# Optimization experiments

Hardware: AMD Instinct MI355X
Metric: run time of the kernel (lower is better)

The kernel has to match this reference:

```python
import jax, jax.numpy as jnp
import numpy as np

B, S, E, H = 2, 2048, 1024, 16
DH = E // H  # 64
EPS = 1e-5


def layer_norm(x, g, b):
    mu = jnp.mean(x, axis=-1, keepdims=True)
    var = jnp.mean(jnp.square(x - mu), axis=-1, keepdims=True)
    return (x - mu) * jax.lax.rsqrt(var + EPS) * g + b


def setup_inputs() -> dict:
    key = jax.random.key(0)
    ks = jax.random.split(key, 12)
    s = lambda fan_in: 1.0 / np.sqrt(fan_in)
    return {
        "x": jax.random.normal(ks[0], (B, S, E), dtype=jnp.float32),
        "ln1_g": jnp.ones((E,), jnp.float32),
        "ln1_b": jnp.zeros((E,), jnp.float32),
        # per-head projections, batched over head axis: [H, E, DH]
        "Wq": jax.random.uniform(ks[1], (H, E, DH), jnp.float32, -s(E), s(E)),
        "Wk": jax.random.uniform(ks[2], (H, E, DH), jnp.float32, -s(E), s(E)),
        "Wv": jax.random.uniform(ks[3], (H, E, DH), jnp.float32, -s(E), s(E)),
        "Wo": jax.random.uniform(ks[4], (H * DH, E), jnp.float32, -s(H * DH), s(H * DH)),
        "bo": jax.random.uniform(ks[5], (E,), jnp.float32, -s(H * DH), s(H * DH)),
        "ln2_g": jnp.ones((E,), jnp.float32),
        "ln2_b": jnp.zeros((E,), jnp.float32),
        "W1": jax.random.uniform(ks[6], (E, 4 * E), jnp.float32, -s(E), s(E)),
        "b1": jax.random.uniform(ks[7], (4 * E,), jnp.float32, -s(E), s(E)),
        "W2": jax.random.uniform(ks[8], (4 * E, E), jnp.float32, -s(4 * E), s(4 * E)),
        "b2": jax.random.uniform(ks[9], (E,), jnp.float32, -s(4 * E), s(4 * E)),
    }


def reference(x, ln1_g, ln1_b, Wq, Wk, Wv, Wo, bo, ln2_g, ln2_b, W1, b1, W2, b2):
    b, s, e = x.shape
    # --- multi-head attention (pre-LN) ---
    h = layer_norm(x, ln1_g, ln1_b)
    q = jnp.einsum("bse,hed->bhsd", h, Wq)
    k = jnp.einsum("bse,hed->bhsd", h, Wk)
    v = jnp.einsum("bse,hed->bhsd", h, Wv)
    # NOTE: original scales by channel**-0.5 (embed_size), not head_size
    scores = jnp.einsum("bhsd,bhtd->bhst", q, k) * (e ** -0.5)
    causal = jnp.tril(jnp.ones((s, s), dtype=bool))
    scores = jnp.where(causal, scores, -jnp.inf)
    attn = jax.nn.softmax(scores, axis=-1)  # dropout is identity in eval
    out = jnp.einsum("bhst,bhtd->bhsd", attn, v)
    out = out.transpose(0, 2, 1, 3).reshape(b, s, -1)  # concat heads: [B,S,H*DH]
    x = x + out @ Wo + bo
    # --- feed-forward (pre-LN) ---
    h2 = layer_norm(x, ln2_g, ln2_b)
    ff = jax.nn.relu(h2 @ W1 + b1) @ W2 + b2
    return x + ff
```

## Files before the change

kernel.cpp:

```cpp
#include <hip/hip_runtime.h>


typedef __bf16 bf16_t;
typedef __attribute__((ext_vector_type(8))) __bf16 bf16x8;
typedef __attribute__((ext_vector_type(4))) __bf16 bf16x4;
typedef __attribute__((ext_vector_type(4))) float f32x4;

#define B_DIM 2
#define S_DIM 2048
#define E_DIM 1024
#define H_DIM 16
#define DH_DIM 64

#define GLD16(gp, lp) __builtin_amdgcn_global_load_lds( \
    (const __attribute__((address_space(1))) void*)(gp), \
    (__attribute__((address_space(3))) void*)(lp), 16, 0, 0)

#define Q_SCALE 0.0450842120f

__global__ __launch_bounds__(256) void ln_kernel(
    const float* __restrict__ x, const float* __restrict__ g,
    const float* __restrict__ bv, bf16_t* __restrict__ out)
{
  const int row = blockIdx.x;
  const int t = threadIdx.x;
  const float* xr = x + (size_t)row * E_DIM;
  float4 v = *(const float4*)&xr[t * 4];
  float s  = v.x + v.y + v.z + v.w;
  float s2 = v.x*v.x + v.y*v.y + v.z*v.z + v.w*v.w;
#pragma unroll
  for (int m = 1; m < 64; m <<= 1) {
    s  += __shfl_xor(s,  m, 64);
    s2 += __shfl_xor(s2, m, 64);
  }
  __shared__ float red[8];
  const int wid = t >> 6, lane = t & 63;
  if (lane == 0) { red[wid] = s; red[4 + wid] = s2; }
  __syncthreads();
  s  = red[0] + red[1] + red[2] + red[3];
  s2 = red[4] + red[5] + red[6] + red[7];
  const float mu  = s * (1.f / E_DIM);
  const float var = s2 * (1.f / E_DIM) - mu * mu;
  const float rs  = rsqrtf(var + 1e-5f);
  float4 gg = *(const float4*)&g[t * 4];
  float4 bb = *(const float4*)&bv[t * 4];
  bf16x4 o;
  o[0] = (bf16_t)((v.x - mu) * rs * gg.x + bb.x);
  o[1] = (bf16_t)((v.y - mu) * rs * gg.y + bb.y);
  o[2] = (bf16_t)((v.z - mu) * rs * gg.z + bb.z);
  o[3] = (bf16_t)((v.w - mu) * rs * gg.w + bb.w);
  *(bf16x4*)&out[(size_t)row * E_DIM + t * 4] = o;
}

__global__ __launch_bounds__(256) void reduce2_ln(
    const float* __restrict__ p, const float* __restrict__ bo,
    const float* __restrict__ x, const float* __restrict__ g,
    const float* __restrict__ bv, float* __restrict__ xmid, bf16_t* __restrict__ h2)
{
  const int row = blockIdx.x;
  const int t = threadIdx.x;
  const size_t off = (size_t)row * E_DIM + t * 4;
  float4 a  = *(const float4*)&p[off];
  float4 b4 = *(const float4*)&p[(size_t)4096 * E_DIM + off];
  float4 xr = *(const float4*)&x[off];
  float4 bo4 = *(const float4*)&bo[t * 4];
  float4 v;
  v.x = a.x + b4.x + xr.x + bo4.x;
  v.y = a.y + b4.y + xr.y + bo4.y;
  v.z = a.z + b4.z + xr.z + bo4.z;
  v.w = a.w + b4.w + xr.w + bo4.w;
  *(float4*)&xmid[off] = v;
  float s  = v.x + v.y + v.z + v.w;
  float s2 = v.x*v.x + v.y*v.y + v.z*v.z + v.w*v.w;
#pragma unroll
  for (int m = 1; m < 64; m <<= 1) {
    s  += __shfl_xor(s,  m, 64);
    s2 += __shfl_xor(s2, m, 64);
  }
  __shared__ float red[8];
  const int wid = t >> 6, lane = t & 63;
  if (lane == 0) { red[wid] = s; red[4 + wid] = s2; }
  __syncthreads();
  s  = red[0] + red[1] + red[2] + red[3];
  s2 = red[4] + red[5] + red[6] + red[7];
  const float mu  = s * (1.f / E_DIM);
  const float var = s2 * (1.f / E_DIM) - mu * mu;
  const float rs  = rsqrtf(var + 1e-5f);
  float4 gg = *(const float4*)&g[t * 4];
  float4 bb = *(const float4*)&bv[t * 4];
  bf16x4 o;
  o[0] = (bf16_t)((v.x - mu) * rs * gg.x + bb.x);
  o[1] = (bf16_t)((v.y - mu) * rs * gg.y + bb.y);
  o[2] = (bf16_t)((v.z - mu) * rs * gg.z + bb.z);
  o[3] = (bf16_t)((v.w - mu) * rs * gg.w + bb.w);
  *(bf16x4*)&h2[off] = o;
}

__global__ __launch_bounds__(256) void reduce4(
    const bf16_t* __restrict__ p0, const bf16_t* __restrict__ p1,
    const bf16_t* __restrict__ p2, const bf16_t* __restrict__ p3,
    const float* __restrict__ b2, const float* __restrict__ xm,
    float* __restrict__ out)
{
  const int row = blockIdx.x;
  const int t = threadIdx.x;
  const size_t off = (size_t)row * E_DIM + t * 4;
  bf16x4 a0 = *(const bf16x4*)&p0[off];
  bf16x4 a1 = *(const bf16x4*)&p1[off];
  bf16x4 a2 = *(const bf16x4*)&p2[off];
  bf16x4 a3 = *(const bf16x4*)&p3[off];
  float4 xr = *(const float4*)&xm[off];
  float4 bb = *(const float4*)&b2[t * 4];
  float4 o;
  o.x = (float)a0[0] + (float)a1[0] + (float)a2[0] + (float)a3[0] + xr.x + bb.x;
  o.y = (float)a0[1] + (float)a1[1] + (float)a2[1] + (float)a3[1] + xr.y + bb.y;
  o.z = (float)a0[2] + (float)a1[2] + (float)a2[2] + (float)a3[2] + xr.z + bb.z;
  o.w = (float)a0[3] + (float)a1[3] + (float)a2[3] + (float)a3[3] + xr.w + bb.w;
  *(float4*)&out[off] = o;
}

__global__ __launch_bounds__(256) void transpose_cast(
    const float* __restrict__ src, bf16_t* __restrict__ dst, int R, int C)
{
  __shared__ float tile[64][65];
  const int c0 = blockIdx.x * 64, r0 = blockIdx.y * 64;
  const int t = threadIdx.x;
  const int rr = t >> 2;
#pragma unroll
  for (int u = 0; u < 4; u++) {
    const int cc = (t & 3) * 4 + u * 16;
    float4 f = *(const float4*)&src[(size_t)(r0 + rr) * C + c0 + cc];
    tile[rr][cc + 0] = f.x; tile[rr][cc + 1] = f.y;
    tile[rr][cc + 2] = f.z; tile[rr][cc + 3] = f.w;
  }
  __syncthreads();
  const int oc = t >> 2;
#pragma unroll
  for (int u = 0; u < 4; u++) {
    const int orr = (t & 3) * 4 + u * 16;
    bf16x4 w;
    w[0] = (bf16_t)tile[orr + 0][oc];
    w[1] = (bf16_t)tile[orr + 1][oc];
    w[2] = (bf16_t)tile[orr + 2][oc];
    w[3] = (bf16_t)tile[orr + 3][oc];
    *(bf16x4*)&dst[(size_t)(c0 + oc) * R + r0 + orr] = w;
  }
}

__global__ __launch_bounds__(256) void qkv_transpose(
    const float* __restrict__ Wq, const float* __restrict__ Wk,
    const float* __restrict__ Wv, bf16_t* __restrict__ dstT)
{
  const int m = blockIdx.y >> 4, h = blockIdx.y & 15;
  const float* src = (m == 0 ? Wq : (m == 1 ? Wk : Wv)) + (size_t)h * E_DIM * DH_DIM;
  const int e0 = blockIdx.x * 64;
  __shared__ float tile[64][65];
  const int t = threadIdx.x;
  const int rr = t >> 2;
#pragma unroll
  for (int u = 0; u < 4; u++) {
    const int cc = (t & 3) * 4 + u * 16;
    float4 f = *(const float4*)&src[(size_t)(e0 + rr) * DH_DIM + cc];
    tile[rr][cc + 0] = f.x; tile[rr][cc + 1] = f.y;
    tile[rr][cc + 2] = f.z; tile[rr][cc + 3] = f.w;
  }
  __syncthreads();
  const int oc = t >> 2;
  const size_t drow = (size_t)(m * 1024 + h * 64 + oc) * E_DIM;
#pragma unroll
  for (int u = 0; u < 4; u++) {
    const int orr = (t & 3) * 4 + u * 16;
    bf16x4 w;
    w[0] = (bf16_t)tile[orr + 0][oc];
    w[1] = (bf16_t)tile[orr + 1][oc];
    w[2] = (bf16_t)tile[orr + 2][oc];
    w[3] = (bf16_t)tile[orr + 3][oc];
    *(bf16x4*)&dstT[drow + e0 + orr] = w;
  }
}

constexpr int EPI_QKV = 0, EPI_BIAS_RELU = 2, EPI_PART_F32 = 3, EPI_PART_B16 = 4;


template <int EPI>
__global__ __launch_bounds__(256) void gemm128_kernel(
    const bf16_t* __restrict__ A, const bf16_t* __restrict__ Bt,
    int M, int N, int Kst, int Klen,
    const float* __restrict__ bias,
    float* __restrict__ outF, bf16_t* __restrict__ outB,
    bf16_t* __restrict__ qo, bf16_t* __restrict__ ko, bf16_t* __restrict__ vo)
{
  __shared__ bf16_t As[3][128 * 32];
  __shared__ bf16_t Bs[3][128 * 32];
  const int gx = gridDim.x;
  const int nwg = gx * gridDim.y;
  int id = blockIdx.y * gx + blockIdx.x;
  id = (id & 7) * (nwg >> 3) + (id >> 3);
  const int m0 = (id % gx) * 128, n0 = (id / gx) * 128;
  const int sp = blockIdx.z;
  A  += (size_t)sp * Klen;
  Bt += (size_t)sp * Klen;

  const int tid = threadIdx.x, lane = tid & 63, wid = tid >> 6;
  const int wr = wid >> 1, wc = wid & 1;
  const int lr = lane & 15, lg = lane >> 4;
  const int halfr = lr >> 1;
  const int sl16 = (((lr & 1) * 4 + lg) ^ halfr) * 16;
  const int baseA = (wr * 32 + halfr) * 128 + sl16;
  const int baseB = (wc * 32 + halfr) * 128 + sl16;

  auto stage = [&](int kt, int buf) {
#pragma unroll
    for (int p = 0; p < 2; p++) {
      const int L = p * 256 + tid;
      const int row2 = L >> 3;
      const int s = (L & 7) ^ (row2 & 7);
      const int r = row2 * 2 + (s >> 2);
      const int u = s & 3;
      char* lb = (char*)&As[buf][0] + (size_t)(p * 256 + wid * 64) * 16;
      char* lbB = (char*)&Bs[buf][0] + (size_t)(p * 256 + wid * 64) * 16;
      GLD16(A  + (size_t)(m0 + r) * Kst + kt * 32 + u * 8, lb);
      GLD16(Bt + (size_t)(n0 + r) * Kst + kt * 32 + u * 8, lbB);
    }
  };

  const f32x4 z4 = {0.f, 0.f, 0.f, 0.f};
  f32x4 acc[4][4];
#pragma unroll
  for (int i = 0; i < 4; i++)
#pragma unroll
    for (int j = 0; j < 4; j++) acc[i][j] = z4;

  const int NT = Klen / 32;
  stage(0, 0);
  stage(1, 1);
  for (int T = 0; T < NT; ++T) {
    const int b = T % 3;
    if (T + 1 < NT) asm volatile("s_waitcnt vmcnt(4)" ::: "memory");
    else            asm volatile("s_waitcnt vmcnt(0)" ::: "memory");
    __builtin_amdgcn_s_barrier();
    if (T + 2 < NT) stage(T + 2, (T + 2) % 3);
    __builtin_amdgcn_sched_barrier(0);

    bf16x8 af[4], bfr[4];
#pragma unroll
    for (int j = 0; j < 4; j++)
      bfr[j] = *(const bf16x8*)((const char*)&Bs[b][0] + baseB + j * 1024);
#pragma unroll
    for (int i = 0; i < 4; i++)
      af[i] = *(const bf16x8*)((const char*)&As[b][0] + baseA + i * 1024);
    __builtin_amdgcn_s_setprio(1);
#pragma unroll
    for (int i = 0; i < 4; i++)
#pragma unroll
      for (int j = 0; j < 4; j++)
        acc[i][j] = __builtin_amdgcn_mfma_f32_16x16x32_bf16(af[i], bfr[j], acc[i][j], 0, 0, 0);
    __builtin_amdgcn_s_setprio(0);
  }

#pragma unroll
  for (int i = 0; i < 4; i++) {
#pragma unroll
    for (int j = 0; j < 4; j++) {
#pragma unroll
      for (int r = 0; r < 4; r++) {
        const int m = m0 + wr * 64 + i * 16 + lg * 4 + r;
        const int n = n0 + wc * 64 + j * 16 + lr;
        const float val = acc[i][j][r];
        if constexpr (EPI == EPI_QKV) {
          const int tsel = n >> 10, h = (n >> 6) & 15, d = n & 63;
          const int b_ = m >> 11, s_ = m & 2047;
          if (tsel == 0)
            qo[((size_t)((b_ * H_DIM + h) * S_DIM + s_)) * DH_DIM + d] = (bf16_t)(val * Q_SCALE);
          else if (tsel == 1)
            ko[((size_t)((b_ * H_DIM + h) * S_DIM + s_)) * DH_DIM + d] = (bf16_t)val;
          else
            vo[((size_t)((b_ * H_DIM + h) * DH_DIM + d)) * S_DIM + s_] = (bf16_t)val;
        } else if constexpr (EPI == EPI_BIAS_RELU) {
          const float u = val + bias[n];
          outB[(size_t)m * N + n] = (bf16_t)(u > 0.f ? u : 0.f);
        } else if constexpr (EPI == EPI_PART_F32) {
          outF[(size_t)sp * M * N + (size_t)m * N + n] = val;
        } else {
          bf16_t* o = sp == 0 ? outB : sp == 1 ? qo : sp == 2 ? ko : vo;
          o[(size_t)m * N + n] = (bf16_t)val;
        }
      }
    }
  }
}

template <int EPI>
__global__ __launch_bounds__(512, 2) void gemm256_kernel(
    const bf16_t* __restrict__ A, const bf16_t* __restrict__ Bt,
    int M, int N, int Kst, int Klen,
    const float* __restrict__ bias,
    float* __restrict__ outF, bf16_t* __restrict__ outB,
    bf16_t* __restrict__ qo, bf16_t* __restrict__ ko, bf16_t* __restrict__ vo)
{
  __shared__ bf16_t As[3][256 * 32];
  __shared__ bf16_t Bs[3][256 * 32];
  const int gx = gridDim.x;
  const int nwg = gx * gridDim.y;
  int id = blockIdx.y * gx + blockIdx.x;
  id = (id & 7) * (nwg >> 3) + (id >> 3);
  const int m0 = (id % gx) * 256, n0 = (id / gx) * 256;
  const int sp = blockIdx.z;
  A  += (size_t)sp * Klen;
  Bt += (size_t)sp * Klen;

  const int tid = threadIdx.x, lane = tid & 63, wid = tid >> 6;
  const int wm = wid >> 2, wn = wid & 3;
  const int lr = lane & 15, lg = lane >> 4;
  const int halfr = lr >> 1;
  const int sl16 = (((lr & 1) * 4 + lg) ^ halfr) * 16;
  const int baseA = (wm * 64 + halfr) * 128 + sl16;
  const int baseB = (wn * 32 + halfr) * 128 + sl16;

  auto stage = [&](int kt, int buf) {
#pragma unroll
    for (int p = 0; p < 2; p++) {
      const int L = p * 512 + tid;
      const int row2 = L >> 3;
      const int s = (L & 7) ^ (row2 & 7);
      const int r = row2 * 2 + (s >> 2);
      const int u = s & 3;
      char* lb = (char*)&As[buf][0] + (size_t)(p * 512 + wid * 64) * 16;
      char* lbB = (char*)&Bs[buf][0] + (size_t)(p * 512 + wid * 64) * 16;
      GLD16(A  + (size_t)(m0 + r) * Kst + kt * 32 + u * 8, lb);
      GLD16(Bt + (size_t)(n0 + r) * Kst + kt * 32 + u * 8, lbB);
    }
  };

  const f32x4 z4 = {0.f, 0.f, 0.f, 0.f};
  f32x4 acc[8][4];
#pragma unroll
  for (int i = 0; i < 8; i++)
#pragma unroll
    for (int j = 0; j < 4; j++) acc[i][j] = z4;

  const int NT = Klen / 32;
  stage(0, 0);
  stage(1, 1);
  for (int T = 0; T < NT; ++T) {
    const int b = T % 3;
    if (T + 1 < NT) asm volatile("s_waitcnt vmcnt(4)" ::: "memory");
    else            asm volatile("s_waitcnt vmcnt(0)" ::: "memory");
    __builtin_amdgcn_s_barrier();
    if (T + 2 < NT) stage(T + 2, (T + 2) % 3);
    __builtin_amdgcn_sched_barrier(0);

    bf16x8 bfr[4];
#pragma unroll
    for (int j = 0; j < 4; j++)
      bfr[j] = *(const bf16x8*)((const char*)&Bs[b][0] + baseB + j * 1024);
    __builtin_amdgcn_s_setprio(1);
#pragma unroll
    for (int i = 0; i < 8; i++) {
      bf16x8 af = *(const bf16x8*)((const char*)&As[b][0] + baseA + i * 1024);
#pragma unroll
      for (int j = 0; j < 4; j++)
        acc[i][j] = __builtin_amdgcn_mfma_f32_16x16x32_bf16(af, bfr[j], acc[i][j], 0, 0, 0);
    }
    __builtin_amdgcn_s_setprio(0);
  }

#pragma unroll
  for (int i = 0; i < 8; i++) {
#pragma unroll
    for (int j = 0; j < 4; j++) {
#pragma unroll
      for (int r = 0; r < 4; r++) {
        const int m = m0 + wm * 128 + i * 16 + lg * 4 + r;
        const int n = n0 + wn * 64 + j * 16 + lr;
        const float val = acc[i][j][r];
        if constexpr (EPI == EPI_BIAS_RELU) {
          const float u = val + bias[n];
          outB[(size_t)m * N + n] = (bf16_t)(u > 0.f ? u : 0.f);
        } else if constexpr (EPI == EPI_PART_F32) {
          outF[(size_t)sp * M * N + (size_t)m * N + n] = val;
        } else if constexpr (EPI == EPI_PART_B16) {
          bf16_t* o = sp == 0 ? outB : sp == 1 ? qo : sp == 2 ? ko : vo;
          o[(size_t)m * N + n] = (bf16_t)val;
        }
      }
    }
  }
}

__global__ __launch_bounds__(256) void attn_kernel(
    const bf16_t* __restrict__ Q, const bf16_t* __restrict__ K,
    const bf16_t* __restrict__ Vt, bf16_t* __restrict__ O,
    bf16_t* __restrict__ Opart, float* __restrict__ mpart, float* __restrict__ lpart)
{
  __shared__ bf16_t Ks[2][64 * 64];
  __shared__ bf16_t Vs[2][64 * 64];
  __shared__ bf16_t Ps[4][16 * 64];

  const int nwg = 80 * gridDim.y;
  int id = blockIdx.y * 80 + blockIdx.x;
  id = (id & 7) * (nwg >> 3) + (id >> 3);
  const int bx = id % 80, bh = id / 80;

  int qt, sp, ns;
  if (bx < 8)       { qt = bx;                sp = 0;            ns = 1; }
  else if (bx < 24) { qt = 8 + ((bx - 8) >> 1);  sp = (bx - 8) & 1;  ns = 2; }
  else if (bx < 48) { const int u = bx - 24; const int q3 = u / 3;
                      qt = 16 + q3;           sp = u - q3 * 3;   ns = 3; }
  else              { const int u = bx - 48;  qt = 24 + (u >> 2); sp = u & 3; ns = 4; }
  const int n = qt + 1;
  const int lo = (sp * n) / ns, hi = ((sp + 1) * n) / ns;

  const int q0b = qt * 64;
  const int tid = threadIdx.x;
  const int wid = tid >> 6, lane = tid & 63;
  const int lr = lane & 15, lg = lane >> 4;
  const int q0w = q0b + wid * 16;

  const bf16_t* Qp = Q  + (size_t)bh * S_DIM * DH_DIM;
  const bf16_t* Kp = K  + (size_t)bh * S_DIM * DH_DIM;
  const bf16_t* Vp = Vt + (size_t)bh * DH_DIM * S_DIM;

  bf16x8 bq[2];
#pragma unroll
  for (int c = 0; c < 2; c++)
    bq[c] = *(const bf16x8*)&Qp[(size_t)(q0w + lr) * DH_DIM + c * 32 + lg * 8];

  const f32x4 z4 = {0.f, 0.f, 0.f, 0.f};
  f32x4 Ot[4];
#pragma unroll
  for (int dt = 0; dt < 4; dt++) Ot[dt] = z4;
  float mrow = -1e30f, lrow = 0.f;

  const int ktr = wid * 8 + (lane >> 3);
  const int ksc = lane & 7;

  auto stageKV = [&](int t0, int buf) {
#pragma unroll
    for (int p = 0; p < 2; p++) {
      const int tr = p * 32 + ktr;
      GLD16(Kp + (size_t)(t0 + tr) * DH_DIM + (ksc ^ (tr & 7)) * 8,
            &Ks[buf][(p * 32 + wid * 8) * 64]);
      GLD16(Vp + (size_t)tr * S_DIM + t0 + (ksc ^ (tr & 7)) * 8,
            &Vs[buf][(p * 32 + wid * 8) * 64]);
    }
  };

  stageKV(lo * 64, 0);

  for (int tc = lo; tc < hi; ++tc) {
    const int cur = (tc - lo) & 1;
    __syncthreads();
    if (tc + 1 < hi) stageKV((tc + 1) * 64, cur ^ 1);

    const int t0 = tc * 64;
    f32x4 sc[4];
    __builtin_amdgcn_s_setprio(1);
#pragma unroll
    for (int j = 0; j < 4; j++) {
      f32x4 s = z4;
      const int t = j * 16 + lr;
#pragma unroll
      for (int c = 0; c < 2; c++) {
        const int kbyte = t * 128 + (((c * 4 + lg) * 16) ^ ((t & 7) << 4));
        bf16x8 ak = *(const bf16x8*)((const char*)&Ks[cur][0] + kbyte);
        s = __builtin_amdgcn_mfma_f32_16x16x32_bf16(ak, bq[c], s, 0, 0, 0);
      }
      sc[j] = s;
    }
    __builtin_amdgcn_s_setprio(0);
    if (tc == qt) {
#pragma unroll
      for (int j = 0; j < 4; j++)
#pragma unroll
        for (int r = 0; r < 4; r++) {
          const int tg = t0 + j * 16 + lg * 4 + r;
          if (tg > q0w + lr) sc[j][r] = -1e30f;
        }
    }
    float mj[4];
#pragma unroll
    for (int j = 0; j < 4; j++)
      mj[j] = fmaxf(fmaxf(sc[j][0], sc[j][1]), fmaxf(sc[j][2], sc[j][3]));
    float tmax = fmaxf(fmaxf(mj[0], mj[1]), fmaxf(mj[2], mj[3]));
    tmax = fmaxf(tmax, __shfl_xor(tmax, 16, 64));
    tmax = fmaxf(tmax, __shfl_xor(tmax, 32, 64));
    if (!__all(tmax <= mrow + 8.f)) {
      const float mnew = fmaxf(mrow, tmax);
      const float fsc = __builtin_exp2f(mrow - mnew);
      mrow = mnew;
      lrow *= fsc;
#pragma unroll
      for (int dt = 0; dt < 4; dt++)
#pragma unroll
        for (int r = 0; r < 4; r++) Ot[dt][r] *= fsc;
    }
    float sj[4];
#pragma unroll
    for (int j = 0; j < 4; j++) {
#pragma unroll
      for (int r = 0; r < 4; r++) sc[j][r] = __builtin_exp2f(sc[j][r] - mrow);
      sj[j] = (sc[j][0] + sc[j][1]) + (sc[j][2] + sc[j][3]);
    }
    float tsum = (sj[0] + sj[1]) + (sj[2] + sj[3]);
    tsum += __shfl_xor(tsum, 16, 64);
    tsum += __shfl_xor(tsum, 32, 64);
    lrow += tsum;

#pragma unroll
    for (int j = 0; j < 4; j++) {
      bf16x4 w;
#pragma unroll
      for (int r = 0; r < 4; r++) w[r] = (bf16_t)sc[j][r];
      const int pbyte = lr * 128 + ((j * 32 + lg * 8) ^ ((lr & 7) << 4));
      *(bf16x4*)((char*)&Ps[wid][0] + pbyte) = w;
    }

    __builtin_amdgcn_s_setprio(1);
#pragma unroll
    for (int c = 0; c < 2; c++) {
      const int abyte = lr * 128 + ((c * 64 + lg * 16) ^ ((lr & 7) << 4));
      bf16x8 pa = *(const bf16x8*)((const char*)&Ps[wid][0] + abyte);
#pragma unroll
      for (int dt = 0; dt < 4; dt++) {
        const int d = dt * 16 + lr;
        const int vbyte = d * 128 + (((c * 4 + lg) * 16) ^ ((d & 7) << 4));
        bf16x8 bv = *(const bf16x8*)((const char*)&Vs[cur][0] + vbyte);
        Ot[dt] = __builtin_amdgcn_mfma_f32_16x16x32_bf16(bv, pa, Ot[dt], 0, 0, 0);
      }
    }
    __builtin_amdgcn_s_setprio(0);
  }

  if (ns == 1) {
    const float linv = 1.f / lrow;
    const int b = bh >> 4, h = bh & 15;
    const int s = q0w + lr;
    const size_t base = ((size_t)(b * S_DIM + s)) * E_DIM + h * DH_DIM;
#pragma unroll
    for (int dt = 0; dt < 4; dt++) {
      bf16x4 w;
#pragma unroll
      for (int r = 0; r < 4; r++) w[r] = (bf16_t)(Ot[dt][r] * linv);
      *(bf16x4*)&O[base + dt * 16 + lg * 4] = w;
    }
  } else {
    const int sbase = (qt < 16) ? 8 + 2 * (qt - 8)
                     : (qt < 24) ? 24 + 3 * (qt - 16) : 48 + 4 * (qt - 24);
    const int slot = bh * 80 + sbase + sp;
    bf16_t* Ob = Opart + (size_t)slot * 64 * 64;
#pragma unroll
    for (int dt = 0; dt < 4; dt++) {
      bf16x4 w;
#pragma unroll
      for (int r = 0; r < 4; r++) w[r] = (bf16_t)Ot[dt][r];
      *(bf16x4*)&Ob[(wid * 16 + lr) * 64 + dt * 16 + lg * 4] = w;
    }
    if (lg == 0) {
      mpart[slot * 64 + wid * 16 + lr] = mrow;
      lpart[slot * 64 + wid * 16 + lr] = lrow;
    }
  }
}

__global__ __launch_bounds__(256) void attn_combine(
    const bf16_t* __restrict__ Opart, const float* __restrict__ mpart,
    const float* __restrict__ lpart, bf16_t* __restrict__ O)
{
  const int qt = 8 + blockIdx.x;
  const int bh = blockIdx.y;
  const int ns = (qt < 16) ? 2 : (qt < 24) ? 3 : 4;
  const int sbase = (qt < 16) ? 8 + 2 * (qt - 8)
                   : (qt < 24) ? 24 + 3 * (qt - 16) : 48 + 4 * (qt - 24);
  const int slot0 = bh * 80 + sbase;
  const int tid = threadIdx.x;
  const int q = tid >> 2, d0 = (tid & 3) * 16;

  float M = -1e30f;
  for (int s = 0; s < ns; s++) M = fmaxf(M, mpart[(slot0 + s) * 64 + q]);
  float L = 0.f;
  float acc[16];
#pragma unroll
  for (int j = 0; j < 16; j++) acc[j] = 0.f;
  for (int s = 0; s < ns; s++) {
    const float w = __builtin_exp2f(mpart[(slot0 + s) * 64 + q] - M);
    L += w * lpart[(slot0 + s) * 64 + q];
    const bf16_t* Ob = Opart + ((size_t)(slot0 + s) * 64 + q) * 64 + d0;
    bf16x8 o0 = *(const bf16x8*)Ob;
    bf16x8 o1 = *(const bf16x8*)(Ob + 8);
#pragma unroll
    for (int j = 0; j < 8; j++) { acc[j] += w * (float)o0[j]; acc[8 + j] += w * (float)o1[j]; }
  }
  const float inv = 1.f / L;
  const int b = bh >> 4, h = bh & 15;
  const int srow = qt * 64 + q;
  bf16_t* out = O + ((size_t)(b * S_DIM + srow)) * E_DIM + h * DH_DIM + d0;
  bf16x8 w0, w1;
#pragma unroll
  for (int j = 0; j < 8; j++) { w0[j] = (bf16_t)(acc[j] * inv); w1[j] = (bf16_t)(acc[8 + j] * inv); }
  *(bf16x8*)out = w0;
  *(bf16x8*)(out + 8) = w1;
}

extern "C" void kernel_launch(void* const* d_in, const int* in_sizes, int n_in,
                              void* d_out, int out_size, void* d_ws, size_t ws_size,
                              hipStream_t stream)
{
  const float* x    = (const float*)d_in[0];
  const float* ln1g = (const float*)d_in[1];
  const float* ln1b = (const float*)d_in[2];
  const float* Wq   = (const float*)d_in[3];
  const float* Wk   = (const float*)d_in[4];
  const float* Wv   = (const float*)d_in[5];
  const float* Wo   = (const float*)d_in[6];
  const float* bo   = (const float*)d_in[7];
  const float* ln2g = (const float*)d_in[8];
  const float* ln2b = (const float*)d_in[9];
  const float* W1   = (const float*)d_in[10];
  const float* b1   = (const float*)d_in[11];
  const float* W2   = (const float*)d_in[12];
  const float* b2   = (const float*)d_in[13];

  char* ws = (char*)d_ws;
  bf16_t* WqkvT = (bf16_t*)(ws + 0);
  bf16_t* WoT   = (bf16_t*)(ws + 6291456);
  bf16_t* W1T   = (bf16_t*)(ws + 8388608);
  bf16_t* W2T   = (bf16_t*)(ws + 16777216);
  bf16_t* h1    = (bf16_t*)(ws + 25165824);
  bf16_t* qb    = (bf16_t*)(ws + 33554432);
  bf16_t* kb    = (bf16_t*)(ws + 41943040);
  bf16_t* vb    = (bf16_t*)(ws + 50331648);
  bf16_t* attnb = (bf16_t*)(ws + 58720256);
  float*  xmid  = (float* )(ws + 67108864);
  bf16_t* h2    = (bf16_t*)(ws + 83886080);
  bf16_t* ff1   = (bf16_t*)(ws + 25165824);
  bf16_t* Opart = (bf16_t*)(ws + 67108864);
  float*  mpart = (float* )(ws + 25165824);
  float*  lpart = (float* )(ws + 25821184);
  float*  po    = (float* )(ws + 25165824);
  bf16_t* pf0   = (bf16_t*)(ws + 0);
  bf16_t* pf1   = (bf16_t*)(ws + 8388608);
  bf16_t* pf2   = (bf16_t*)(ws + 58720256);
  bf16_t* pf3   = (bf16_t*)(ws + 83886080);

  qkv_transpose<<<dim3(16, 48), 256, 0, stream>>>(Wq, Wk, Wv, WqkvT);
  transpose_cast<<<dim3(16, 16), 256, 0, stream>>>(Wo, WoT, 1024, 1024);
  transpose_cast<<<dim3(64, 16), 256, 0, stream>>>(W1, W1T, 1024, 4096);
  transpose_cast<<<dim3(16, 64), 256, 0, stream>>>(W2, W2T, 4096, 1024);

  ln_kernel<<<4096, 256, 0, stream>>>(x, ln1g, ln1b, h1);
  gemm128_kernel<EPI_QKV><<<dim3(32, 24, 1), 256, 0, stream>>>(
      h1, WqkvT, 4096, 3072, 1024, 1024, nullptr,
      nullptr, nullptr, qb, kb, vb);
  attn_kernel<<<dim3(80, 32), 256, 0, stream>>>(qb, kb, vb, attnb, Opart, mpart, lpart);
  attn_combine<<<dim3(24, 32), 256, 0, stream>>>(Opart, mpart, lpart, attnb);
  gemm128_kernel<EPI_PART_F32><<<dim3(32, 8, 2), 256, 0, stream>>>(
      attnb, WoT, 4096, 1024, 1024, 512, nullptr,
      po, nullptr, nullptr, nullptr, nullptr);
  reduce2_ln<<<4096, 256, 0, stream>>>(po, bo, x, ln2g, ln2b, xmid, h2);
  gemm256_kernel<EPI_BIAS_RELU><<<dim3(16, 16, 1), 512, 0, stream>>>(
      h2, W1T, 4096, 4096, 1024, 1024, b1,
      nullptr, ff1, nullptr, nullptr, nullptr);
  gemm256_kernel<EPI_PART_B16><<<dim3(16, 4, 4), 512, 0, stream>>>(
      ff1, W2T, 4096, 1024, 4096, 1024, nullptr,
      nullptr, pf0, pf1, pf2, pf3);
  reduce4<<<4096, 256, 0, stream>>>(pf0, pf1, pf2, pf3, b2, xmid, (float*)d_out);

  (void)in_sizes; (void)n_in; (void)out_size; (void)ws_size;
}
```

Before: 278.4 us.

## Process 128-row query tiles per attention block and drop the 256-tile GEMM

The attention kernel now gives each wave 32 query rows (two 16-row MFMA tiles) instead of 16. Each staged K/V tile is therefore reused for twice the work, and the grid, split slots and combine indexing are halved to match. Separately, the 256x256 GEMM kernel is removed and both FFN GEMMs run through the existing 128-tile GEMM with larger grids. This trades fewer K/V loads and barriers per query row for higher register pressure in attention, and possibly lower arithmetic intensity in the FFN GEMMs.

```diff
diff --git a/kernel.cpp b/kernel.cpp
--- a/kernel.cpp
+++ b/kernel.cpp
@@ -290,104 +290,6 @@
   }
 }
 
-template <int EPI>
-__global__ __launch_bounds__(512, 2) void gemm256_kernel(
-    const bf16_t* __restrict__ A, const bf16_t* __restrict__ Bt,
-    int M, int N, int Kst, int Klen,
-    const float* __restrict__ bias,
-    float* __restrict__ outF, bf16_t* __restrict__ outB,
-    bf16_t* __restrict__ qo, bf16_t* __restrict__ ko, bf16_t* __restrict__ vo)
-{
-  __shared__ bf16_t As[3][256 * 32];
-  __shared__ bf16_t Bs[3][256 * 32];
-  const int gx = gridDim.x;
-  const int nwg = gx * gridDim.y;
-  int id = blockIdx.y * gx + blockIdx.x;
-  id = (id & 7) * (nwg >> 3) + (id >> 3);
-  const int m0 = (id % gx) * 256, n0 = (id / gx) * 256;
-  const int sp = blockIdx.z;
-  A  += (size_t)sp * Klen;
-  Bt += (size_t)sp * Klen;
-
-  const int tid = threadIdx.x, lane = tid & 63, wid = tid >> 6;
-  const int wm = wid >> 2, wn = wid & 3;
-  const int lr = lane & 15, lg = lane >> 4;
-  const int halfr = lr >> 1;
-  const int sl16 = (((lr & 1) * 4 + lg) ^ halfr) * 16;
-  const int baseA = (wm * 64 + halfr) * 128 + sl16;
-  const int baseB = (wn * 32 + halfr) * 128 + sl16;
-
-  auto stage = [&](int kt, int buf) {
-#pragma unroll
-    for (int p = 0; p < 2; p++) {
-      const int L = p * 512 + tid;
-      const int row2 = L >> 3;
-      const int s = (L & 7) ^ (row2 & 7);
-      const int r = row2 * 2 + (s >> 2);
-      const int u = s & 3;
-      char* lb = (char*)&As[buf][0] + (size_t)(p * 512 + wid * 64) * 16;
-      char* lbB = (char*)&Bs[buf][0] + (size_t)(p * 512 + wid * 64) * 16;
-      GLD16(A  + (size_t)(m0 + r) * Kst + kt * 32 + u * 8, lb);
-      GLD16(Bt + (size_t)(n0 + r) * Kst + kt * 32 + u * 8, lbB);
-    }
-  };
-
-  const f32x4 z4 = {0.f, 0.f, 0.f, 0.f};
-  f32x4 acc[8][4];
-#pragma unroll
-  for (int i = 0; i < 8; i++)
-#pragma unroll
-    for (int j = 0; j < 4; j++) acc[i][j] = z4;
-
-  const int NT = Klen / 32;
-  stage(0, 0);
-  stage(1, 1);
-  for (int T = 0; T < NT; ++T) {
-    const int b = T % 3;
-    if (T + 1 < NT) asm volatile("s_waitcnt vmcnt(4)" ::: "memory");
-    else            asm volatile("s_waitcnt vmcnt(0)" ::: "memory");
-    __builtin_amdgcn_s_barrier();
-    if (T + 2 < NT) stage(T + 2, (T + 2) % 3);
-    __builtin_amdgcn_sched_barrier(0);
-
-    bf16x8 bfr[4];
-#pragma unroll
-    for (int j = 0; j < 4; j++)
-      bfr[j] = *(const bf16x8*)((const char*)&Bs[b][0] + baseB + j * 1024);
-    __builtin_amdgcn_s_setprio(1);
-#pragma unroll
-    for (int i = 0; i < 8; i++) {
-      bf16x8 af = *(const bf16x8*)((const char*)&As[b][0] + baseA + i * 1024);
-#pragma unroll
-      for (int j = 0; j < 4; j++)
-        acc[i][j] = __builtin_amdgcn_mfma_f32_16x16x32_bf16(af, bfr[j], acc[i][j], 0, 0, 0);
-    }
-    __builtin_amdgcn_s_setprio(0);
-  }
-
-#pragma unroll
-  for (int i = 0; i < 8; i++) {
-#pragma unroll
-    for (int j = 0; j < 4; j++) {
-#pragma unroll
-      for (int r = 0; r < 4; r++) {
-        const int m = m0 + wm * 128 + i * 16 + lg * 4 + r;
-        const int n = n0 + wn * 64 + j * 16 + lr;
-        const float val = acc[i][j][r];
-        if constexpr (EPI == EPI_BIAS_RELU) {
-          const float u = val + bias[n];
-          outB[(size_t)m * N + n] = (bf16_t)(u > 0.f ? u : 0.f);
-        } else if constexpr (EPI == EPI_PART_F32) {
-          outF[(size_t)sp * M * N + (size_t)m * N + n] = val;
-        } else if constexpr (EPI == EPI_PART_B16) {
-          bf16_t* o = sp == 0 ? outB : sp == 1 ? qo : sp == 2 ? ko : vo;
-          o[(size_t)m * N + n] = (bf16_t)val;
-        }
-      }
-    }
-  }
-}
-
 __global__ __launch_bounds__(256) void attn_kernel(
     const bf16_t* __restrict__ Q, const bf16_t* __restrict__ K,
     const bf16_t* __restrict__ Vt, bf16_t* __restrict__ O,
@@ -395,42 +297,44 @@
 {
   __shared__ bf16_t Ks[2][64 * 64];
   __shared__ bf16_t Vs[2][64 * 64];
-  __shared__ bf16_t Ps[4][16 * 64];
-
-  const int nwg = 80 * gridDim.y;
-  int id = blockIdx.y * 80 + blockIdx.x;
+  __shared__ bf16_t Ps[4][2][16 * 64];
+
+  const int nwg = 40 * gridDim.y;
+  int id = blockIdx.y * 40 + blockIdx.x;
   id = (id & 7) * (nwg >> 3) + (id >> 3);
-  const int bx = id % 80, bh = id / 80;
-
-  int qt, sp, ns;
-  if (bx < 8)       { qt = bx;                sp = 0;            ns = 1; }
-  else if (bx < 24) { qt = 8 + ((bx - 8) >> 1);  sp = (bx - 8) & 1;  ns = 2; }
-  else if (bx < 48) { const int u = bx - 24; const int q3 = u / 3;
-                      qt = 16 + q3;           sp = u - q3 * 3;   ns = 3; }
-  else              { const int u = bx - 48;  qt = 24 + (u >> 2); sp = u & 3; ns = 4; }
-  const int n = qt + 1;
-  const int lo = (sp * n) / ns, hi = ((sp + 1) * n) / ns;
-
-  const int q0b = qt * 64;
+  const int bx = id % 40, bh = id / 40;
+
+  int q2, sp, ns;
+  if (bx < 4)       { q2 = bx;                      sp = 0;          ns = 1; }
+  else if (bx < 12) { const int u = bx - 4;  q2 = 4 + (u >> 1);  sp = u & 1;  ns = 2; }
+  else if (bx < 24) { const int u = bx - 12; const int q3 = u / 3;
+                      q2 = 8 + q3;                  sp = u - q3 * 3; ns = 3; }
+  else              { const int u = bx - 24; q2 = 12 + (u >> 2); sp = u & 3;  ns = 4; }
+  const int n2 = 2 * q2 + 2;
+  const int lo = (sp * n2) / ns, hi = ((sp + 1) * n2) / ns;
+
   const int tid = threadIdx.x;
   const int wid = tid >> 6, lane = tid & 63;
   const int lr = lane & 15, lg = lane >> 4;
-  const int q0w = q0b + wid * 16;
+  const int q0w = q2 * 128 + wid * 32;
 
   const bf16_t* Qp = Q  + (size_t)bh * S_DIM * DH_DIM;
   const bf16_t* Kp = K  + (size_t)bh * S_DIM * DH_DIM;
   const bf16_t* Vp = Vt + (size_t)bh * DH_DIM * S_DIM;
 
-  bf16x8 bq[2];
-#pragma unroll
-  for (int c = 0; c < 2; c++)
-    bq[c] = *(const bf16x8*)&Qp[(size_t)(q0w + lr) * DH_DIM + c * 32 + lg * 8];
+  bf16x8 bq0[2], bq1[2];
+#pragma unroll
+  for (int c = 0; c < 2; c++) {
+    bq0[c] = *(const bf16x8*)&Qp[(size_t)(q0w + lr) * DH_DIM + c * 32 + lg * 8];
+    bq1[c] = *(const bf16x8*)&Qp[(size_t)(q0w + 16 + lr) * DH_DIM + c * 32 + lg * 8];
+  }
 
   const f32x4 z4 = {0.f, 0.f, 0.f, 0.f};
-  f32x4 Ot[4];
-#pragma unroll
-  for (int dt = 0; dt < 4; dt++) Ot[dt] = z4;
-  float mrow = -1e30f, lrow = 0.f;
+  f32x4 Ot0[4], Ot1[4];
+#pragma unroll
+  for (int dt = 0; dt < 4; dt++) { Ot0[dt] = z4; Ot1[dt] = z4; }
+  float mrow0 = -1e30f, lrow0 = 0.f;
+  float mrow1 = -1e30f, lrow1 = 0.f;
 
   const int ktr = wid * 8 + (lane >> 3);
   const int ksc = lane & 7;
@@ -454,111 +358,168 @@
     if (tc + 1 < hi) stageKV((tc + 1) * 64, cur ^ 1);
 
     const int t0 = tc * 64;
-    f32x4 sc[4];
+    f32x4 s0[4], s1[4];
     __builtin_amdgcn_s_setprio(1);
 #pragma unroll
     for (int j = 0; j < 4; j++) {
-      f32x4 s = z4;
+      f32x4 a = z4, b = z4;
       const int t = j * 16 + lr;
 #pragma unroll
       for (int c = 0; c < 2; c++) {
         const int kbyte = t * 128 + (((c * 4 + lg) * 16) ^ ((t & 7) << 4));
         bf16x8 ak = *(const bf16x8*)((const char*)&Ks[cur][0] + kbyte);
-        s = __builtin_amdgcn_mfma_f32_16x16x32_bf16(ak, bq[c], s, 0, 0, 0);
-      }
-      sc[j] = s;
+        a = __builtin_amdgcn_mfma_f32_16x16x32_bf16(ak, bq0[c], a, 0, 0, 0);
+        b = __builtin_amdgcn_mfma_f32_16x16x32_bf16(ak, bq1[c], b, 0, 0, 0);
+      }
+      s0[j] = a; s1[j] = b;
     }
     __builtin_amdgcn_s_setprio(0);
-    if (tc == qt) {
+    if (tc >= 2 * q2) {
 #pragma unroll
       for (int j = 0; j < 4; j++)
 #pragma unroll
         for (int r = 0; r < 4; r++) {
           const int tg = t0 + j * 16 + lg * 4 + r;
-          if (tg > q0w + lr) sc[j][r] = -1e30f;
+          if (tg > q0w + lr)      s0[j][r] = -1e30f;
+          if (tg > q0w + 16 + lr) s1[j][r] = -1e30f;
         }
     }
-    float mj[4];
-#pragma unroll
-    for (int j = 0; j < 4; j++)
-      mj[j] = fmaxf(fmaxf(sc[j][0], sc[j][1]), fmaxf(sc[j][2], sc[j][3]));
-    float tmax = fmaxf(fmaxf(mj[0], mj[1]), fmaxf(mj[2], mj[3]));
-    tmax = fmaxf(tmax, __shfl_xor(tmax, 16, 64));
-    tmax = fmaxf(tmax, __shfl_xor(tmax, 32, 64));
-    if (!__all(tmax <= mrow + 8.f)) {
-      const float mnew = fmaxf(mrow, tmax);
-      const float fsc = __builtin_exp2f(mrow - mnew);
-      mrow = mnew;
-      lrow *= fsc;
-#pragma unroll
-      for (int dt = 0; dt < 4; dt++)
-#pragma unroll
-        for (int r = 0; r < 4; r++) Ot[dt][r] *= fsc;
-    }
-    float sj[4];
-#pragma unroll
-    for (int j = 0; j < 4; j++) {
-#pragma unroll
-      for (int r = 0; r < 4; r++) sc[j][r] = __builtin_exp2f(sc[j][r] - mrow);
-      sj[j] = (sc[j][0] + sc[j][1]) + (sc[j][2] + sc[j][3]);
-    }
-    float tsum = (sj[0] + sj[1]) + (sj[2] + sj[3]);
-    tsum += __shfl_xor(tsum, 16, 64);
-    tsum += __shfl_xor(tsum, 32, 64);
-    lrow += tsum;
-
-#pragma unroll
-    for (int j = 0; j < 4; j++) {
-      bf16x4 w;
-#pragma unroll
-      for (int r = 0; r < 4; r++) w[r] = (bf16_t)sc[j][r];
-      const int pbyte = lr * 128 + ((j * 32 + lg * 8) ^ ((lr & 7) << 4));
-      *(bf16x4*)((char*)&Ps[wid][0] + pbyte) = w;
+    {
+      float mj[4];
+#pragma unroll
+      for (int j = 0; j < 4; j++)
+        mj[j] = fmaxf(fmaxf(s0[j][0], s0[j][1]), fmaxf(s0[j][2], s0[j][3]));
+      float tmax = fmaxf(fmaxf(mj[0], mj[1]), fmaxf(mj[2], mj[3]));
+      tmax = fmaxf(tmax, __shfl_xor(tmax, 16, 64));
+      tmax = fmaxf(tmax, __shfl_xor(tmax, 32, 64));
+      if (!__all(tmax <= mrow0 + 8.f)) {
+        const float mnew = fmaxf(mrow0, tmax);
+        const float fsc = __builtin_exp2f(mrow0 - mnew);
+        mrow0 = mnew; lrow0 *= fsc;
+#pragma unroll
+        for (int dt = 0; dt < 4; dt++)
+#pragma unroll
+          for (int r = 0; r < 4; r++) Ot0[dt][r] *= fsc;
+      }
+      float sj[4];
+#pragma unroll
+      for (int j = 0; j < 4; j++) {
+#pragma unroll
+        for (int r = 0; r < 4; r++) s0[j][r] = __builtin_exp2f(s0[j][r] - mrow0);
+        sj[j] = (s0[j][0] + s0[j][1]) + (s0[j][2] + s0[j][3]);
+      }
+      float tsum = (sj[0] + sj[1]) + (sj[2] + sj[3]);
+      tsum += __shfl_xor(tsum, 16, 64);
+      tsum += __shfl_xor(tsum, 32, 64);
+      lrow0 += tsum;
+#pragma unroll
+      for (int j = 0; j < 4; j++) {
+        bf16x4 w;
+#pragma unroll
+        for (int r = 0; r < 4; r++) w[r] = (bf16_t)s0[j][r];
+        const int pbyte = lr * 128 + ((j * 32 + lg * 8) ^ ((lr & 7) << 4));
+        *(bf16x4*)((char*)&Ps[wid][0][0] + pbyte) = w;
+      }
+    }
+    {
+      float mj[4];
+#pragma unroll
+      for (int j = 0; j < 4; j++)
+        mj[j] = fmaxf(fmaxf(s1[j][0], s1[j][1]), fmaxf(s1[j][2], s1[j][3]));
+      float tmax = fmaxf(fmaxf(mj[0], mj[1]), fmaxf(mj[2], mj[3]));
+      tmax = fmaxf(tmax, __shfl_xor(tmax, 16, 64));
+      tmax = fmaxf(tmax, __shfl_xor(tmax, 32, 64));
+      if (!__all(tmax <= mrow1 + 8.f)) {
+        const float mnew = fmaxf(mrow1, tmax);
+        const float fsc = __builtin_exp2f(mrow1 - mnew);
+        mrow1 = mnew; lrow1 *= fsc;
+#pragma unroll
+        for (int dt = 0; dt < 4; dt++)
+#pragma unroll
+          for (int r = 0; r < 4; r++) Ot1[dt][r] *= fsc;
+      }
+      float sj[4];
+#pragma unroll
+      for (int j = 0; j < 4; j++) {
+#pragma unroll
+        for (int r = 0; r < 4; r++) s1[j][r] = __builtin_exp2f(s1[j][r] - mrow1);
+        sj[j] = (s1[j][0] + s1[j][1]) + (s1[j][2] + s1[j][3]);
+      }
+      float tsum = (sj[0] + sj[1]) + (sj[2] + sj[3]);
+      tsum += __shfl_xor(tsum, 16, 64);
+      tsum += __shfl_xor(tsum, 32, 64);
+      lrow1 += tsum;
+#pragma unroll
+      for (int j = 0; j < 4; j++) {
+        bf16x4 w;
+#pragma unroll
+        for (int r = 0; r < 4; r++) w[r] = (bf16_t)s1[j][r];
+        const int pbyte = lr * 128 + ((j * 32 + lg * 8) ^ ((lr & 7) << 4));
+        *(bf16x4*)((char*)&Ps[wid][1][0] + pbyte) = w;
+      }
     }
 
     __builtin_amdgcn_s_setprio(1);
 #pragma unroll
     for (int c = 0; c < 2; c++) {
       const int abyte = lr * 128 + ((c * 64 + lg * 16) ^ ((lr & 7) << 4));
-      bf16x8 pa = *(const bf16x8*)((const char*)&Ps[wid][0] + abyte);
+      bf16x8 pa0 = *(const bf16x8*)((const char*)&Ps[wid][0][0] + abyte);
+      bf16x8 pa1 = *(const bf16x8*)((const char*)&Ps[wid][1][0] + abyte);
 #pragma unroll
       for (int dt = 0; dt < 4; dt++) {
         const int d = dt * 16 + lr;
         const int vbyte = d * 128 + (((c * 4 + lg) * 16) ^ ((d & 7) << 4));
         bf16x8 bv = *(const bf16x8*)((const char*)&Vs[cur][0] + vbyte);
-        Ot[dt] = __builtin_amdgcn_mfma_f32_16x16x32_bf16(bv, pa, Ot[dt], 0, 0, 0);
+        Ot0[dt] = __builtin_amdgcn_mfma_f32_16x16x32_bf16(bv, pa0, Ot0[dt], 0, 0, 0);
+        Ot1[dt] = __builtin_amdgcn_mfma_f32_16x16x32_bf16(bv, pa1, Ot1[dt], 0, 0, 0);
       }
     }
     __builtin_amdgcn_s_setprio(0);
   }
 
   if (ns == 1) {
-    const float linv = 1.f / lrow;
     const int b = bh >> 4, h = bh & 15;
-    const int s = q0w + lr;
-    const size_t base = ((size_t)(b * S_DIM + s)) * E_DIM + h * DH_DIM;
+    {
+      const float linv = 1.f / lrow0;
+      const size_t base = ((size_t)(b * S_DIM + q0w + lr)) * E_DIM + h * DH_DIM;
+#pragma unroll
+      for (int dt = 0; dt < 4; dt++) {
+        bf16x4 w;
+#pragma unroll
+        for (int r = 0; r < 4; r++) w[r] = (bf16_t)(Ot0[dt][r] * linv);
+        *(bf16x4*)&O[base + dt * 16 + lg * 4] = w;
+      }
+    }
+    {
+      const float linv = 1.f / lrow1;
+      const size_t base = ((size_t)(b * S_DIM + q0w + 16 + lr)) * E_DIM + h * DH_DIM;
+#pragma unroll
+      for (int dt = 0; dt < 4; dt++) {
+        bf16x4 w;
+#pragma unroll
+        for (int r = 0; r < 4; r++) w[r] = (bf16_t)(Ot1[dt][r] * linv);
+        *(bf16x4*)&O[base + dt * 16 + lg * 4] = w;
+      }
+    }
+  } else {
+    const int sbase = (q2 < 8) ? 4 + 2 * (q2 - 4)
+                     : (q2 < 12) ? 12 + 3 * (q2 - 8) : 24 + 4 * (q2 - 12);
+    const int psl = bh * 36 + (sbase - 4) + sp;
+    bf16_t* Ob = Opart + (size_t)psl * 128 * 64;
+    const int row0 = wid * 32 + lr, row1 = row0 + 16;
 #pragma unroll
     for (int dt = 0; dt < 4; dt++) {
-      bf16x4 w;
-#pragma unroll
-      for (int r = 0; r < 4; r++) w[r] = (bf16_t)(Ot[dt][r] * linv);
-      *(bf16x4*)&O[base + dt * 16 + lg * 4] = w;
-    }
-  } else {
-    const int sbase = (qt < 16) ? 8 + 2 * (qt - 8)
-                     : (qt < 24) ? 24 + 3 * (qt - 16) : 48 + 4 * (qt - 24);
-    const int slot = bh * 80 + sbase + sp;
-    bf16_t* Ob = Opart + (size_t)slot * 64 * 64;
-#pragma unroll
-    for (int dt = 0; dt < 4; dt++) {
-      bf16x4 w;
-#pragma unroll
-      for (int r = 0; r < 4; r++) w[r] = (bf16_t)Ot[dt][r];
-      *(bf16x4*)&Ob[(wid * 16 + lr) * 64 + dt * 16 + lg * 4] = w;
+      bf16x4 w0, w1;
+#pragma unroll
+      for (int r = 0; r < 4; r++) { w0[r] = (bf16_t)Ot0[dt][r]; w1[r] = (bf16_t)Ot1[dt][r]; }
+      *(bf16x4*)&Ob[row0 * 64 + dt * 16 + lg * 4] = w0;
+      *(bf16x4*)&Ob[row1 * 64 + dt * 16 + lg * 4] = w1;
     }
     if (lg == 0) {
-      mpart[slot * 64 + wid * 16 + lr] = mrow;
-      lpart[slot * 64 + wid * 16 + lr] = lrow;
+      mpart[psl * 128 + row0] = mrow0;
+      lpart[psl * 128 + row0] = lrow0;
+      mpart[psl * 128 + row1] = mrow1;
+      lpart[psl * 128 + row1] = lrow1;
     }
   }
 }
@@ -567,25 +528,27 @@
     const bf16_t* __restrict__ Opart, const float* __restrict__ mpart,
     const float* __restrict__ lpart, bf16_t* __restrict__ O)
 {
-  const int qt = 8 + blockIdx.x;
+  const int q2 = 4 + (blockIdx.x >> 1);
+  const int half = blockIdx.x & 1;
   const int bh = blockIdx.y;
-  const int ns = (qt < 16) ? 2 : (qt < 24) ? 3 : 4;
-  const int sbase = (qt < 16) ? 8 + 2 * (qt - 8)
-                   : (qt < 24) ? 24 + 3 * (qt - 16) : 48 + 4 * (qt - 24);
-  const int slot0 = bh * 80 + sbase;
+  const int ns = (q2 < 8) ? 2 : (q2 < 12) ? 3 : 4;
+  const int sbase = (q2 < 8) ? 4 + 2 * (q2 - 4)
+                   : (q2 < 12) ? 12 + 3 * (q2 - 8) : 24 + 4 * (q2 - 12);
+  const int psl0 = bh * 36 + (sbase - 4);
   const int tid = threadIdx.x;
   const int q = tid >> 2, d0 = (tid & 3) * 16;
+  const int row = half * 64 + q;
 
   float M = -1e30f;
-  for (int s = 0; s < ns; s++) M = fmaxf(M, mpart[(slot0 + s) * 64 + q]);
+  for (int s = 0; s < ns; s++) M = fmaxf(M, mpart[(psl0 + s) * 128 + row]);
   float L = 0.f;
   float acc[16];
 #pragma unroll
   for (int j = 0; j < 16; j++) acc[j] = 0.f;
   for (int s = 0; s < ns; s++) {
-    const float w = __builtin_exp2f(mpart[(slot0 + s) * 64 + q] - M);
-    L += w * lpart[(slot0 + s) * 64 + q];
-    const bf16_t* Ob = Opart + ((size_t)(slot0 + s) * 64 + q) * 64 + d0;
+    const float w = __builtin_exp2f(mpart[(psl0 + s) * 128 + row] - M);
+    L += w * lpart[(psl0 + s) * 128 + row];
+    const bf16_t* Ob = Opart + ((size_t)(psl0 + s) * 128 + row) * 64 + d0;
     bf16x8 o0 = *(const bf16x8*)Ob;
     bf16x8 o1 = *(const bf16x8*)(Ob + 8);
 #pragma unroll
@@ -593,7 +556,7 @@
   }
   const float inv = 1.f / L;
   const int b = bh >> 4, h = bh & 15;
-  const int srow = qt * 64 + q;
+  const int srow = q2 * 128 + row;
   bf16_t* out = O + ((size_t)(b * S_DIM + srow)) * E_DIM + h * DH_DIM + d0;
   bf16x8 w0, w1;
 #pragma unroll
@@ -636,7 +599,7 @@
   bf16_t* ff1   = (bf16_t*)(ws + 25165824);
   bf16_t* Opart = (bf16_t*)(ws + 67108864);
   float*  mpart = (float* )(ws + 25165824);
-  float*  lpart = (float* )(ws + 25821184);
+  float*  lpart = (float* )(ws + 25755648);
   float*  po    = (float* )(ws + 25165824);
   bf16_t* pf0   = (bf16_t*)(ws + 0);
   bf16_t* pf1   = (bf16_t*)(ws + 8388608);
@@ -652,16 +615,16 @@
   gemm128_kernel<EPI_QKV><<<dim3(32, 24, 1), 256, 0, stream>>>(
       h1, WqkvT, 4096, 3072, 1024, 1024, nullptr,
       nullptr, nullptr, qb, kb, vb);
-  attn_kernel<<<dim3(80, 32), 256, 0, stream>>>(qb, kb, vb, attnb, Opart, mpart, lpart);
+  attn_kernel<<<dim3(40, 32), 256, 0, stream>>>(qb, kb, vb, attnb, Opart, mpart, lpart);
   attn_combine<<<dim3(24, 32), 256, 0, stream>>>(Opart, mpart, lpart, attnb);
   gemm128_kernel<EPI_PART_F32><<<dim3(32, 8, 2), 256, 0, stream>>>(
       attnb, WoT, 4096, 1024, 1024, 512, nullptr,
       po, nullptr, nullptr, nullptr, nullptr);
   reduce2_ln<<<4096, 256, 0, stream>>>(po, bo, x, ln2g, ln2b, xmid, h2);
-  gemm256_kernel<EPI_BIAS_RELU><<<dim3(16, 16, 1), 512, 0, stream>>>(
+  gemm128_kernel<EPI_BIAS_RELU><<<dim3(32, 32, 1), 256, 0, stream>>>(
       h2, W1T, 4096, 4096, 1024, 1024, b1,
       nullptr, ff1, nullptr, nullptr, nullptr);
-  gemm256_kernel<EPI_PART_B16><<<dim3(16, 4, 4), 512, 0, stream>>>(
+  gemm128_kernel<EPI_PART_B16><<<dim3(32, 8, 4), 256, 0, stream>>>(
       ff1, W2T, 4096, 1024, 4096, 1024, nullptr,
       nullptr, pf0, pf1, pf2, pf3);
   reduce4<<<4096, 256, 0, stream>>>(pf0, pf1, pf2, pf3, b2, xmid, (float*)d_out);
```

Measured after the change: 298.2 us. +7.1%, slower.
